# Performance work log

Measured on AMD Instinct MI355X. Metric: run time of the kernel, lower is better.

Reference implementation:

```python
import jax, jax.numpy as jnp
import numpy as np

B, T, I, H, TGT = 256, 4096, 8, 32, 8


def setup_inputs() -> dict:
    key = jax.random.key(0)
    ks = jax.random.split(key, 6)
    return {
        "inputs": jax.random.normal(ks[0], (B, T, I), jnp.float32),
        "encode_weights": jax.random.normal(ks[1], (H, I), jnp.float32) * 0.3,   # xavier-ish
        "w_ih": jax.random.normal(ks[2], (3 * H, H), jnp.float32) * 0.1,        # GRU weight_ih_l0
        "w_hh": jax.random.normal(ks[3], (3 * H, H), jnp.float32) * 0.1,        # GRU weight_hh_l0
        "b_ih": jax.random.normal(ks[4], (3 * H,), jnp.float32) * 0.1,
        "b_hh": jax.random.normal(ks[5], (3 * H,), jnp.float32) * 0.1,
    }


def _gru(gx_t, w_hh, b_hh, h0):
    # gx_t: time-major input-gate pre-activations [T, B, 3H]; PyTorch GRU math:
    # r = sig(gx_r + gh_r); z = sig(gx_z + gh_z); n = tanh(gx_n + r*gh_n); h = (1-z)*n + z*h
    Hd = h0.shape[-1]
    def step(h, gx):
        gh = h @ w_hh.T + b_hh                      # [B, 3H]
        r = jax.nn.sigmoid(gx[..., :Hd] + gh[..., :Hd])
        z = jax.nn.sigmoid(gx[..., Hd:2 * Hd] + gh[..., Hd:2 * Hd])
        n = jnp.tanh(gx[..., 2 * Hd:] + r * gh[..., 2 * Hd:])
        h_new = (1.0 - z) * n + z * h
        return h_new, h_new
    _, hs = jax.lax.scan(step, h0, gx_t)            # hs: [T, B, H]
    return hs


def reference(inputs, encode_weights, w_ih, w_hh, b_ih, b_hh):
    # encode = F.linear(inputs, encode_weights)
    encode = jnp.einsum('bti,hi->bth', inputs, encode_weights)      # [B, T, H]
    gx = jnp.einsum('bth,gh->btg', encode, w_ih) + b_ih             # [B, T, 3H]
    gx_t = jnp.swapaxes(gx, 0, 1)                                   # [T, B, 3H]
    h0 = jnp.zeros((inputs.shape[0], encode_weights.shape[0]), inputs.dtype)
    latents = jnp.swapaxes(_gru(gx_t, w_hh, b_hh, h0), 0, 1)        # [B, T, H]
    # tied decoder: F.linear(latents, encode_weights[:, :target_size].T)
    outputs = jnp.einsum('bth,ho->bto', latents, encode_weights[:, :TGT])
    return outputs, latents
```

## Files before the change

kernel.cpp:

```cpp
#include <hip/hip_runtime.h>
#include <hip/hip_bf16.h>
#include <cstdint>
#include <cstddef>

#define Bsz  256
#define Tn   4096
#define In   8
#define Hn   32
#define TGTn 8

#define ALPHA (-1.44269504088896341f)
#define BETA  ( 2.88539008177792682f)

#if __has_builtin(__builtin_amdgcn_exp2f)
__device__ __forceinline__ float exp2f_fast(float x) { return __builtin_amdgcn_exp2f(x); }
#else
__device__ __forceinline__ float exp2f_fast(float x) { return __expf(x * 0.69314718056f); }
#endif
__device__ __forceinline__ float rcpf(float x) { return __builtin_amdgcn_rcpf(x); }

__device__ __forceinline__ float half_sum(float x) {
    auto r = __builtin_amdgcn_permlane32_swap(__float_as_int(x), __float_as_int(x),
                                              false, false);
    return __int_as_float((int)r[0]) + __int_as_float((int)r[1]);
}

__global__ void fuse_wih_kernel(const float* __restrict__ w_ih,
                                const float* __restrict__ E,
                                float* __restrict__ Wf) {
    int tid = threadIdx.x;
    int g = tid >> 3, i = tid & 7;
    float acc = 0.f;
#pragma unroll
    for (int k = 0; k < Hn; ++k)
        acc = fmaf(w_ih[g * Hn + k], E[k * In + i], acc);
    Wf[g * In + i] = acc;
}

#define GRU_STEP(XA, XB, XRA, XRB, DO_REFILL)                                        \
  {                                                                                  \
             \
    float ar = br_h, az = bz_h, anx = bxn_f, anh = bhn_h;                            \
    ar  = fmaf(XA.x, wxr0, ar);  ar  = fmaf(XA.y, wxr1, ar);                         \
    ar  = fmaf(XA.z, wxr2, ar);  ar  = fmaf(XA.w, wxr3, ar);                         \
    ar  = fmaf(XB.x, wxr4, ar);  ar  = fmaf(XB.y, wxr5, ar);                         \
    ar  = fmaf(XB.z, wxr6, ar);  ar  = fmaf(XB.w, wxr7, ar);                         \
    az  = fmaf(XA.x, wxz0, az);  az  = fmaf(XA.y, wxz1, az);                         \
    az  = fmaf(XA.z, wxz2, az);  az  = fmaf(XA.w, wxz3, az);                         \
    az  = fmaf(XB.x, wxz4, az);  az  = fmaf(XB.y, wxz5, az);                         \
    az  = fmaf(XB.z, wxz6, az);  az  = fmaf(XB.w, wxz7, az);                         \
    anx = fmaf(XA.x, wxn0, anx); anx = fmaf(XA.y, wxn1, anx);                        \
    anx = fmaf(XA.z, wxn2, anx); anx = fmaf(XA.w, wxn3, anx);                        \
    anx = fmaf(XB.x, wxn4, anx); anx = fmaf(XB.y, wxn5, anx);                        \
    anx = fmaf(XB.z, wxn6, anx); anx = fmaf(XB.w, wxn7, anx);                        \
                                                    \
    ar = fmaf(H0,  wr0,  ar);  az = fmaf(H0,  wz0,  az);  anh = fmaf(H0,  wn0,  anh);\
    ar = fmaf(H1,  wr1,  ar);  az = fmaf(H1,  wz1,  az);  anh = fmaf(H1,  wn1,  anh);\
    ar = fmaf(H2,  wr2,  ar);  az = fmaf(H2,  wz2,  az);  anh = fmaf(H2,  wn2,  anh);\
    ar = fmaf(H3,  wr3,  ar);  az = fmaf(H3,  wz3,  az);  anh = fmaf(H3,  wn3,  anh);\
    ar = fmaf(H4,  wr4,  ar);  az = fmaf(H4,  wz4,  az);  anh = fmaf(H4,  wn4,  anh);\
    ar = fmaf(H5,  wr5,  ar);  az = fmaf(H5,  wz5,  az);  anh = fmaf(H5,  wn5,  anh);\
    ar = fmaf(H6,  wr6,  ar);  az = fmaf(H6,  wz6,  az);  anh = fmaf(H6,  wn6,  anh);\
    ar = fmaf(H7,  wr7,  ar);  az = fmaf(H7,  wz7,  az);  anh = fmaf(H7,  wn7,  anh);\
    ar = fmaf(H8,  wr8,  ar);  az = fmaf(H8,  wz8,  az);  anh = fmaf(H8,  wn8,  anh);\
    ar = fmaf(H9,  wr9,  ar);  az = fmaf(H9,  wz9,  az);  anh = fmaf(H9,  wn9,  anh);\
    ar = fmaf(H10, wr10, ar);  az = fmaf(H10, wz10, az);  anh = fmaf(H10, wn10, anh);\
    ar = fmaf(H11, wr11, ar);  az = fmaf(H11, wz11, az);  anh = fmaf(H11, wn11, anh);\
    ar = fmaf(H12, wr12, ar);  az = fmaf(H12, wz12, az);  anh = fmaf(H12, wn12, anh);\
    ar = fmaf(H13, wr13, ar);  az = fmaf(H13, wz13, az);  anh = fmaf(H13, wn13, anh);\
    ar = fmaf(H14, wr14, ar);  az = fmaf(H14, wz14, az);  anh = fmaf(H14, wn14, anh);\
    ar = fmaf(H15, wr15, ar);  az = fmaf(H15, wz15, az);  anh = fmaf(H15, wn15, anh);\
    float cr  = half_sum(ar);                           \
    float cz  = half_sum(az);                                                        \
    float chn = half_sum(anh);                          \
    float r = rcpf(1.f + exp2f_fast(cr));                                            \
    float z = rcpf(1.f + exp2f_fast(cz));                                            \
    float e = exp2f_fast(__builtin_fmaf(r, chn, anx));                               \
    float u = rcpf(e + 1.f);                                                         \
    float n = __builtin_fmaf(-2.f, u, 1.f);                                          \
    hj = __builtin_fmaf(z, hj - n, n);                                               \
    lds_h[j] = hj;                               \
    latb_u[j] = hj;                                                                  \
    latb_u += Hn;                                               \
    if (DO_REFILL) {                                                                 \
        XRA = *(const float4*)refp;                                                  \
        XRB = *(const float4*)(refp + 4);                                            \
        refp += In;                                             \
    }                                                                                \
               \
    {                                                                                \
        float4 q0 = *(const float4*)&lds_h[grp * 16 + 0];                            \
        float4 q1 = *(const float4*)&lds_h[grp * 16 + 4];                            \
        float4 q2 = *(const float4*)&lds_h[grp * 16 + 8];                            \
        float4 q3 = *(const float4*)&lds_h[grp * 16 + 12];                           \
        H0  = q0.x; H1  = q0.y; H2  = q0.z; H3  = q0.w;                              \
        H4  = q1.x; H5  = q1.y; H6  = q1.z; H7  = q1.w;                              \
        H8  = q2.x; H9  = q2.y; H10 = q2.z; H11 = q2.w;                              \
        H12 = q3.x; H13 = q3.y; H14 = q3.z; H15 = q3.w;                              \
    }                                                                                \
  }

#define KEEP(v) asm volatile("" : "+v"(v))
__attribute__((amdgpu_flat_work_group_size(64, 64), amdgpu_waves_per_eu(1, 1)))
__global__ void gru_kernel(const float* __restrict__ x,
                           const float* __restrict__ Wf,
                           const float* __restrict__ w_hh,
                           const float* __restrict__ b_ih,
                           const float* __restrict__ b_hh,
                           float* __restrict__ latents) {
    __shared__ __align__(16) float lds_h[Hn];

    const int lane = threadIdx.x & 63;
    const int grp  = lane >> 5;
    const int j    = lane & 31;
    const int b    = blockIdx.x;

    float wr0,wr1,wr2,wr3,wr4,wr5,wr6,wr7,wr8,wr9,wr10,wr11,wr12,wr13,wr14,wr15;
    float wz0,wz1,wz2,wz3,wz4,wz5,wz6,wz7,wz8,wz9,wz10,wz11,wz12,wz13,wz14,wz15;
    float wn0,wn1,wn2,wn3,wn4,wn5,wn6,wn7,wn8,wn9,wn10,wn11,wn12,wn13,wn14,wn15;
#define LOADW(M)                                                                  \
    {                                                                             \
        const int c = grp * 16 + M;                                               \
        wr##M = ALPHA * w_hh[(0*Hn + j)*Hn + c];                                  \
        wz##M = ALPHA * w_hh[(1*Hn + j)*Hn + c];                                  \
        wn##M = BETA  * w_hh[(2*Hn + j)*Hn + c];                                  \
        KEEP(wr##M); KEEP(wz##M); KEEP(wn##M);                                    \
    }
    LOADW(0) LOADW(1) LOADW(2)  LOADW(3)  LOADW(4)  LOADW(5)  LOADW(6)  LOADW(7)
    LOADW(8) LOADW(9) LOADW(10) LOADW(11) LOADW(12) LOADW(13) LOADW(14) LOADW(15)
#undef LOADW

    float wxr0,wxr1,wxr2,wxr3,wxr4,wxr5,wxr6,wxr7;
    float wxz0,wxz1,wxz2,wxz3,wxz4,wxz5,wxz6,wxz7;
    float wxn0,wxn1,wxn2,wxn3,wxn4,wxn5,wxn6,wxn7;
#define LOADX(I)                                                                  \
    wxr##I = 0.5f * ALPHA * Wf[(0*Hn + j)*In + I];                                \
    wxz##I = 0.5f * ALPHA * Wf[(1*Hn + j)*In + I];                                \
    wxn##I = BETA         * Wf[(2*Hn + j)*In + I];                                \
    KEEP(wxr##I); KEEP(wxz##I); KEEP(wxn##I);
    LOADX(0) LOADX(1) LOADX(2) LOADX(3) LOADX(4) LOADX(5) LOADX(6) LOADX(7)
#undef LOADX

    float br_h  = 0.5f * ALPHA * (b_ih[j]        + b_hh[j]);
    float bz_h  = 0.5f * ALPHA * (b_ih[Hn + j]   + b_hh[Hn + j]);
    float bxn_f = BETA * b_ih[2*Hn + j];
    float bhn_h = 0.5f * BETA * b_hh[2*Hn + j];
    KEEP(br_h); KEEP(bz_h); KEEP(bxn_f); KEEP(bhn_h);

    const float* xb   = x + (size_t)b * Tn * In;
    float* latb_u     = latents + (size_t)b * Tn * Hn;
    const float* refp = xb + 4 * In;

    float hj = 0.f;
    float H0=0.f,H1=0.f,H2=0.f,H3=0.f,H4=0.f,H5=0.f,H6=0.f,H7=0.f,
          H8=0.f,H9=0.f,H10=0.f,H11=0.f,H12=0.f,H13=0.f,H14=0.f,H15=0.f;

    float4 a0 = *(const float4*)&xb[0*In], b0 = *(const float4*)&xb[0*In + 4];
    float4 a1 = *(const float4*)&xb[1*In], b1 = *(const float4*)&xb[1*In + 4];
    float4 a2 = *(const float4*)&xb[2*In], b2 = *(const float4*)&xb[2*In + 4];
    float4 a3 = *(const float4*)&xb[3*In], b3 = *(const float4*)&xb[3*In + 4];

#pragma unroll 1
    for (int s0 = 0; s0 < Tn - 4; s0 += 4) {
        GRU_STEP(a0, b0, a0, b0, true)
        GRU_STEP(a1, b1, a1, b1, true)
        GRU_STEP(a2, b2, a2, b2, true)
        GRU_STEP(a3, b3, a3, b3, true)
    }
    GRU_STEP(a0, b0, a0, b0, false)
    GRU_STEP(a1, b1, a1, b1, false)
    GRU_STEP(a2, b2, a2, b2, false)
    GRU_STEP(a3, b3, a3, b3, false)
}
#undef KEEP

__global__ void decode_kernel(const float* __restrict__ lat,
                              const float* __restrict__ E,
                              float* __restrict__ out) {
    __shared__ float ldsE[Hn * TGTn];
    int tid = threadIdx.x;
    if (tid < Hn * TGTn) ldsE[tid] = E[tid];
    __syncthreads();
    size_t idx = (size_t)blockIdx.x * 256 + tid;
    int o      = (int)(idx & (TGTn - 1));
    size_t row = idx >> 3;
    const float* lrow = lat + row * Hn;
    float acc = 0.f;
#pragma unroll
    for (int h = 0; h < Hn; ++h)
        acc = fmaf(lrow[h], ldsE[h * TGTn + o], acc);
    out[idx] = acc;
}

extern "C" void kernel_launch(void* const* d_in, const int* in_sizes, int n_in,
                              void* d_out, int out_size, void* d_ws, size_t ws_size,
                              hipStream_t stream) {
    const float* x    = (const float*)d_in[0];
    const float* E    = (const float*)d_in[1];
    const float* w_ih = (const float*)d_in[2];
    const float* w_hh = (const float*)d_in[3];
    const float* b_ih = (const float*)d_in[4];
    const float* b_hh = (const float*)d_in[5];

    float* out = (float*)d_out;
    float* lat = out + (size_t)Bsz * Tn * TGTn;
    float* Wf  = (float*)d_ws;

    fuse_wih_kernel<<<1, 768, 0, stream>>>(w_ih, E, Wf);
    gru_kernel<<<Bsz, 64, 0, stream>>>(x, Wf, w_hh, b_ih, b_hh, lat);
    decode_kernel<<<(Bsz * Tn * TGTn) / 256, 256, 0, stream>>>(lat, E, out);
}
```

Measured before the change: 1.143 ms.

## Replace LDS hidden-state broadcast with DPP row-rotate FMAs and permlane swaps

The per-step hidden-state exchange no longer goes through shared memory (an LDS write followed by four float4 reads). Each lane now holds one hidden value and the recurrent matvec uses v_fmac_f32 with DPP row_ror operands, so the value moves across lanes inside the FMA. Lanes are remapped and the w_hh weights are pre-permuted to match, with permlane16/permlane32 swaps doing the reductions and the redistribution of h. This targets LDS latency on the serial critical path of the recurrence, at the cost of inline asm with hand-placed s_nop hazards and a tricky lane mapping that could be wrong.

```diff
diff --git a/kernel.cpp b/kernel.cpp
--- a/kernel.cpp
+++ b/kernel.cpp
@@ -19,11 +19,26 @@
 #endif
 __device__ __forceinline__ float rcpf(float x) { return __builtin_amdgcn_rcpf(x); }
 
-__device__ __forceinline__ float half_sum(float x) {
-    auto r = __builtin_amdgcn_permlane32_swap(__float_as_int(x), __float_as_int(x),
+template<int N>
+__device__ __forceinline__ float dpp_ror(float x) {
+    int xi = __float_as_int(x);
+    int r = __builtin_amdgcn_update_dpp(xi, xi, 0x120 + N, 0xF, 0xF, false);
+    return __int_as_float(r);
+}
+
+__device__ __forceinline__ float halfsum16(float x) {
+    auto r = __builtin_amdgcn_permlane16_swap(__float_as_int(x), __float_as_int(x),
                                               false, false);
     return __int_as_float((int)r[0]) + __int_as_float((int)r[1]);
 }
+
+#define FMAC_DPP(acc, h, w, N)                                                       \
+    asm volatile("v_fmac_f32 %0, %1, %2 row_ror:" #N " row_mask:0xf bank_mask:0xf"   \
+                 : "+v"(acc) : "v"(h), "v"(w))
+#define FMAC_DPP_FIRST(acc, h, w, N)                                                 \
+    asm volatile("s_nop 1\n\t"                                                       \
+                 "v_fmac_f32 %0, %1, %2 row_ror:" #N " row_mask:0xf bank_mask:0xf"   \
+                 : "+v"(acc) : "v"(h), "v"(w))
 
 __global__ void fuse_wih_kernel(const float* __restrict__ w_ih,
                                 const float* __restrict__ E,
@@ -37,9 +52,14 @@
     Wf[g * In + i] = acc;
 }
 
+#define HROT3(N)                                                                     \
+    FMAC_DPP(ar,  hsrc, whr##N, N);                                                  \
+    FMAC_DPP(az,  hsrc, whz##N, N);                                                  \
+    FMAC_DPP(anh, hsrc, whn##N, N);
+
 #define GRU_STEP(XA, XB, XRA, XRB, DO_REFILL)                                        \
   {                                                                                  \
-             \
+                       \
     float ar = br_h, az = bz_h, anx = bxn_f, anh = bhn_h;                            \
     ar  = fmaf(XA.x, wxr0, ar);  ar  = fmaf(XA.y, wxr1, ar);                         \
     ar  = fmaf(XA.z, wxr2, ar);  ar  = fmaf(XA.w, wxr3, ar);                         \
@@ -53,50 +73,39 @@
     anx = fmaf(XA.z, wxn2, anx); anx = fmaf(XA.w, wxn3, anx);                        \
     anx = fmaf(XB.x, wxn4, anx); anx = fmaf(XB.y, wxn5, anx);                        \
     anx = fmaf(XB.z, wxn6, anx); anx = fmaf(XB.w, wxn7, anx);                        \
-                                                    \
-    ar = fmaf(H0,  wr0,  ar);  az = fmaf(H0,  wz0,  az);  anh = fmaf(H0,  wn0,  anh);\
-    ar = fmaf(H1,  wr1,  ar);  az = fmaf(H1,  wz1,  az);  anh = fmaf(H1,  wn1,  anh);\
-    ar = fmaf(H2,  wr2,  ar);  az = fmaf(H2,  wz2,  az);  anh = fmaf(H2,  wn2,  anh);\
-    ar = fmaf(H3,  wr3,  ar);  az = fmaf(H3,  wz3,  az);  anh = fmaf(H3,  wn3,  anh);\
-    ar = fmaf(H4,  wr4,  ar);  az = fmaf(H4,  wz4,  az);  anh = fmaf(H4,  wn4,  anh);\
-    ar = fmaf(H5,  wr5,  ar);  az = fmaf(H5,  wz5,  az);  anh = fmaf(H5,  wn5,  anh);\
-    ar = fmaf(H6,  wr6,  ar);  az = fmaf(H6,  wz6,  az);  anh = fmaf(H6,  wn6,  anh);\
-    ar = fmaf(H7,  wr7,  ar);  az = fmaf(H7,  wz7,  az);  anh = fmaf(H7,  wn7,  anh);\
-    ar = fmaf(H8,  wr8,  ar);  az = fmaf(H8,  wz8,  az);  anh = fmaf(H8,  wn8,  anh);\
-    ar = fmaf(H9,  wr9,  ar);  az = fmaf(H9,  wz9,  az);  anh = fmaf(H9,  wn9,  anh);\
-    ar = fmaf(H10, wr10, ar);  az = fmaf(H10, wz10, az);  anh = fmaf(H10, wn10, anh);\
-    ar = fmaf(H11, wr11, ar);  az = fmaf(H11, wz11, az);  anh = fmaf(H11, wn11, anh);\
-    ar = fmaf(H12, wr12, ar);  az = fmaf(H12, wz12, az);  anh = fmaf(H12, wn12, anh);\
-    ar = fmaf(H13, wr13, ar);  az = fmaf(H13, wz13, az);  anh = fmaf(H13, wn13, anh);\
-    ar = fmaf(H14, wr14, ar);  az = fmaf(H14, wz14, az);  anh = fmaf(H14, wn14, anh);\
-    ar = fmaf(H15, wr15, ar);  az = fmaf(H15, wz15, az);  anh = fmaf(H15, wn15, anh);\
-    float cr  = half_sum(ar);                           \
-    float cz  = half_sum(az);                                                        \
-    float chn = half_sum(anh);                          \
+            \
+    ar  = fmaf(hsrc, whr0, ar);                                                      \
+    az  = fmaf(hsrc, whz0, az);                                                      \
+    anh = fmaf(hsrc, whn0, anh);                                                     \
+    FMAC_DPP_FIRST(ar, hsrc, whr1, 1);                                               \
+    FMAC_DPP(az,  hsrc, whz1, 1);                                                    \
+    FMAC_DPP(anh, hsrc, whn1, 1);                                                    \
+    HROT3(2)  HROT3(3)  HROT3(4)  HROT3(5)  HROT3(6)  HROT3(7)  HROT3(8)             \
+    HROT3(9)  HROT3(10) HROT3(11) HROT3(12) HROT3(13) HROT3(14) HROT3(15)            \
+    float cr  = halfsum16(ar);                           \
+    float cz  = halfsum16(az);                                                       \
+    float chn = halfsum16(anh);                          \
     float r = rcpf(1.f + exp2f_fast(cr));                                            \
     float z = rcpf(1.f + exp2f_fast(cz));                                            \
     float e = exp2f_fast(__builtin_fmaf(r, chn, anx));                               \
     float u = rcpf(e + 1.f);                                                         \
     float n = __builtin_fmaf(-2.f, u, 1.f);                                          \
     hj = __builtin_fmaf(z, hj - n, n);                                               \
-    lds_h[j] = hj;                               \
-    latb_u[j] = hj;                                                                  \
+               \
+    {                                                                                \
+        auto rr = __builtin_amdgcn_permlane32_swap(__float_as_int(hj),               \
+                                                   __float_as_int(hj),               \
+                                                   false, false);                    \
+        float s0 = __int_as_float((int)rr[0]);                                       \
+        float s1 = __int_as_float((int)rr[1]);                                       \
+        hsrc = pickr1 ? s1 : s0;                                                     \
+    }                                                                                \
+    latb_u[j] = hj;                            \
     latb_u += Hn;                                               \
     if (DO_REFILL) {                                                                 \
         XRA = *(const float4*)refp;                                                  \
         XRB = *(const float4*)(refp + 4);                                            \
         refp += In;                                             \
-    }                                                                                \
-               \
-    {                                                                                \
-        float4 q0 = *(const float4*)&lds_h[grp * 16 + 0];                            \
-        float4 q1 = *(const float4*)&lds_h[grp * 16 + 4];                            \
-        float4 q2 = *(const float4*)&lds_h[grp * 16 + 8];                            \
-        float4 q3 = *(const float4*)&lds_h[grp * 16 + 12];                           \
-        H0  = q0.x; H1  = q0.y; H2  = q0.z; H3  = q0.w;                              \
-        H4  = q1.x; H5  = q1.y; H6  = q1.z; H7  = q1.w;                              \
-        H8  = q2.x; H9  = q2.y; H10 = q2.z; H11 = q2.w;                              \
-        H12 = q3.x; H13 = q3.y; H14 = q3.z; H15 = q3.w;                              \
     }                                                                                \
   }
 
@@ -108,23 +117,45 @@
                            const float* __restrict__ b_ih,
                            const float* __restrict__ b_hh,
                            float* __restrict__ latents) {
-    __shared__ __align__(16) float lds_h[Hn];
-
-    const int lane = threadIdx.x & 63;
-    const int grp  = lane >> 5;
-    const int j    = lane & 31;
-    const int b    = blockIdx.x;
-
-    float wr0,wr1,wr2,wr3,wr4,wr5,wr6,wr7,wr8,wr9,wr10,wr11,wr12,wr13,wr14,wr15;
-    float wz0,wz1,wz2,wz3,wz4,wz5,wz6,wz7,wz8,wz9,wz10,wz11,wz12,wz13,wz14,wz15;
-    float wn0,wn1,wn2,wn3,wn4,wn5,wn6,wn7,wn8,wn9,wn10,wn11,wn12,wn13,wn14,wn15;
+    const int lane   = threadIdx.x & 63;
+    const int rowpar = (lane >> 4) & 1;
+    const int j      = (lane & 15) | ((lane >> 1) & 16);
+    const int b      = blockIdx.x;
+
+    int rho[16];
+    {
+        float q = (float)(lane & 15);
+        rho[0]  = lane & 15;
+        rho[1]  = (int)dpp_ror<1>(q);   rho[2]  = (int)dpp_ror<2>(q);
+        rho[3]  = (int)dpp_ror<3>(q);   rho[4]  = (int)dpp_ror<4>(q);
+        rho[5]  = (int)dpp_ror<5>(q);   rho[6]  = (int)dpp_ror<6>(q);
+        rho[7]  = (int)dpp_ror<7>(q);   rho[8]  = (int)dpp_ror<8>(q);
+        rho[9]  = (int)dpp_ror<9>(q);   rho[10] = (int)dpp_ror<10>(q);
+        rho[11] = (int)dpp_ror<11>(q);  rho[12] = (int)dpp_ror<12>(q);
+        rho[13] = (int)dpp_ror<13>(q);  rho[14] = (int)dpp_ror<14>(q);
+        rho[15] = (int)dpp_ror<15>(q);
+    }
+    bool pickr1;
+    {
+        float t = (float)lane;
+        auto rr = __builtin_amdgcn_permlane32_swap(__float_as_int(t),
+                                                   __float_as_int(t),
+                                                   false, false);
+        bool r0_own    = ((int)__int_as_float((int)rr[0]) == lane);
+        bool use_swap  = (rowpar != ((lane >> 5) & 1));
+        pickr1 = (use_swap == r0_own);
+    }
+
+    float whr0,whr1,whr2,whr3,whr4,whr5,whr6,whr7,whr8,whr9,whr10,whr11,whr12,whr13,whr14,whr15;
+    float whz0,whz1,whz2,whz3,whz4,whz5,whz6,whz7,whz8,whz9,whz10,whz11,whz12,whz13,whz14,whz15;
+    float whn0,whn1,whn2,whn3,whn4,whn5,whn6,whn7,whn8,whn9,whn10,whn11,whn12,whn13,whn14,whn15;
 #define LOADW(M)                                                                  \
     {                                                                             \
-        const int c = grp * 16 + M;                                               \
-        wr##M = ALPHA * w_hh[(0*Hn + j)*Hn + c];                                  \
-        wz##M = ALPHA * w_hh[(1*Hn + j)*Hn + c];                                  \
-        wn##M = BETA  * w_hh[(2*Hn + j)*Hn + c];                                  \
-        KEEP(wr##M); KEEP(wz##M); KEEP(wn##M);                                    \
+        const int c = rowpar * 16 + rho[M];                                       \
+        whr##M = ALPHA * w_hh[(0*Hn + j)*Hn + c];                                 \
+        whz##M = ALPHA * w_hh[(1*Hn + j)*Hn + c];                                 \
+        whn##M = BETA  * w_hh[(2*Hn + j)*Hn + c];                                 \
+        KEEP(whr##M); KEEP(whz##M); KEEP(whn##M);                                 \
     }
     LOADW(0) LOADW(1) LOADW(2)  LOADW(3)  LOADW(4)  LOADW(5)  LOADW(6)  LOADW(7)
     LOADW(8) LOADW(9) LOADW(10) LOADW(11) LOADW(12) LOADW(13) LOADW(14) LOADW(15)
@@ -152,8 +183,7 @@
     const float* refp = xb + 4 * In;
 
     float hj = 0.f;
-    float H0=0.f,H1=0.f,H2=0.f,H3=0.f,H4=0.f,H5=0.f,H6=0.f,H7=0.f,
-          H8=0.f,H9=0.f,H10=0.f,H11=0.f,H12=0.f,H13=0.f,H14=0.f,H15=0.f;
+    float hsrc = 0.f;
 
     float4 a0 = *(const float4*)&xb[0*In], b0 = *(const float4*)&xb[0*In + 4];
     float4 a1 = *(const float4*)&xb[1*In], b1 = *(const float4*)&xb[1*In + 4];
```

New measurement: 959.6 us, median of 2. 16.1% less time.

## Map two batch rows per wave with full-length hidden dot per lane

Applied to the files above, without the earlier changes.

Each wave now processes two batch elements: a 32-lane half per row, with each lane computing the full 32-wide recurrent dot product for its hidden unit. This removes the permlane32 swap half-sum reduction from every step. The input-gate pre-activation for the next step is computed after the hidden-state store, taking it off the recurrence's critical path. In exchange each lane issues twice as many recurrent FMAs and LDS reads per step, holds twice as many weight registers, and only half as many workgroups are launched.

```diff
diff --git a/kernel.cpp b/kernel.cpp
--- a/kernel.cpp
+++ b/kernel.cpp
@@ -18,12 +18,6 @@
 __device__ __forceinline__ float exp2f_fast(float x) { return __expf(x * 0.69314718056f); }
 #endif
 __device__ __forceinline__ float rcpf(float x) { return __builtin_amdgcn_rcpf(x); }
-
-__device__ __forceinline__ float half_sum(float x) {
-    auto r = __builtin_amdgcn_permlane32_swap(__float_as_int(x), __float_as_int(x),
-                                              false, false);
-    return __int_as_float((int)r[0]) + __int_as_float((int)r[1]);
-}
 
 __global__ void fuse_wih_kernel(const float* __restrict__ w_ih,
                                 const float* __restrict__ E,
@@ -37,70 +31,73 @@
     Wf[g * In + i] = acc;
 }
 
-#define GRU_STEP(XA, XB, XRA, XRB, DO_REFILL)                                        \
+#define KEEP(v) asm volatile("" : "+v"(v))
+
+#define H_FMA(K)                                                                     \
+    ar  = fmaf(H##K, wr##K, ar);                                                     \
+    az  = fmaf(H##K, wz##K, az);                                                     \
+    anh = fmaf(H##K, wn##K, anh);
+
+#define RELOAD_H()                                                                   \
   {                                                                                  \
-             \
-    float ar = br_h, az = bz_h, anx = bxn_f, anh = bhn_h;                            \
-    ar  = fmaf(XA.x, wxr0, ar);  ar  = fmaf(XA.y, wxr1, ar);                         \
-    ar  = fmaf(XA.z, wxr2, ar);  ar  = fmaf(XA.w, wxr3, ar);                         \
-    ar  = fmaf(XB.x, wxr4, ar);  ar  = fmaf(XB.y, wxr5, ar);                         \
-    ar  = fmaf(XB.z, wxr6, ar);  ar  = fmaf(XB.w, wxr7, ar);                         \
-    az  = fmaf(XA.x, wxz0, az);  az  = fmaf(XA.y, wxz1, az);                         \
-    az  = fmaf(XA.z, wxz2, az);  az  = fmaf(XA.w, wxz3, az);                         \
-    az  = fmaf(XB.x, wxz4, az);  az  = fmaf(XB.y, wxz5, az);                         \
-    az  = fmaf(XB.z, wxz6, az);  az  = fmaf(XB.w, wxz7, az);                         \
-    anx = fmaf(XA.x, wxn0, anx); anx = fmaf(XA.y, wxn1, anx);                        \
-    anx = fmaf(XA.z, wxn2, anx); anx = fmaf(XA.w, wxn3, anx);                        \
-    anx = fmaf(XB.x, wxn4, anx); anx = fmaf(XB.y, wxn5, anx);                        \
-    anx = fmaf(XB.z, wxn6, anx); anx = fmaf(XB.w, wxn7, anx);                        \
-                                                    \
-    ar = fmaf(H0,  wr0,  ar);  az = fmaf(H0,  wz0,  az);  anh = fmaf(H0,  wn0,  anh);\
-    ar = fmaf(H1,  wr1,  ar);  az = fmaf(H1,  wz1,  az);  anh = fmaf(H1,  wn1,  anh);\
-    ar = fmaf(H2,  wr2,  ar);  az = fmaf(H2,  wz2,  az);  anh = fmaf(H2,  wn2,  anh);\
-    ar = fmaf(H3,  wr3,  ar);  az = fmaf(H3,  wz3,  az);  anh = fmaf(H3,  wn3,  anh);\
-    ar = fmaf(H4,  wr4,  ar);  az = fmaf(H4,  wz4,  az);  anh = fmaf(H4,  wn4,  anh);\
-    ar = fmaf(H5,  wr5,  ar);  az = fmaf(H5,  wz5,  az);  anh = fmaf(H5,  wn5,  anh);\
-    ar = fmaf(H6,  wr6,  ar);  az = fmaf(H6,  wz6,  az);  anh = fmaf(H6,  wn6,  anh);\
-    ar = fmaf(H7,  wr7,  ar);  az = fmaf(H7,  wz7,  az);  anh = fmaf(H7,  wn7,  anh);\
-    ar = fmaf(H8,  wr8,  ar);  az = fmaf(H8,  wz8,  az);  anh = fmaf(H8,  wn8,  anh);\
-    ar = fmaf(H9,  wr9,  ar);  az = fmaf(H9,  wz9,  az);  anh = fmaf(H9,  wn9,  anh);\
-    ar = fmaf(H10, wr10, ar);  az = fmaf(H10, wz10, az);  anh = fmaf(H10, wn10, anh);\
-    ar = fmaf(H11, wr11, ar);  az = fmaf(H11, wz11, az);  anh = fmaf(H11, wn11, anh);\
-    ar = fmaf(H12, wr12, ar);  az = fmaf(H12, wz12, az);  anh = fmaf(H12, wn12, anh);\
-    ar = fmaf(H13, wr13, ar);  az = fmaf(H13, wz13, az);  anh = fmaf(H13, wn13, anh);\
-    ar = fmaf(H14, wr14, ar);  az = fmaf(H14, wz14, az);  anh = fmaf(H14, wn14, anh);\
-    ar = fmaf(H15, wr15, ar);  az = fmaf(H15, wz15, az);  anh = fmaf(H15, wn15, anh);\
-    float cr  = half_sum(ar);                           \
-    float cz  = half_sum(az);                                                        \
-    float chn = half_sum(anh);                          \
-    float r = rcpf(1.f + exp2f_fast(cr));                                            \
-    float z = rcpf(1.f + exp2f_fast(cz));                                            \
-    float e = exp2f_fast(__builtin_fmaf(r, chn, anx));                               \
+    float4 q0 = *(const float4*)&lds_h[hbase + 0];                                   \
+    float4 q1 = *(const float4*)&lds_h[hbase + 4];                                   \
+    float4 q2 = *(const float4*)&lds_h[hbase + 8];                                   \
+    float4 q3 = *(const float4*)&lds_h[hbase + 12];                                  \
+    float4 q4 = *(const float4*)&lds_h[hbase + 16];                                  \
+    float4 q5 = *(const float4*)&lds_h[hbase + 20];                                  \
+    float4 q6 = *(const float4*)&lds_h[hbase + 24];                                  \
+    float4 q7 = *(const float4*)&lds_h[hbase + 28];                                  \
+    H0 =q0.x; H1 =q0.y; H2 =q0.z; H3 =q0.w;  H4 =q1.x; H5 =q1.y; H6 =q1.z; H7 =q1.w; \
+    H8 =q2.x; H9 =q2.y; H10=q2.z; H11=q2.w;  H12=q3.x; H13=q3.y; H14=q3.z; H15=q3.w; \
+    H16=q4.x; H17=q4.y; H18=q4.z; H19=q4.w;  H20=q5.x; H21=q5.y; H22=q5.z; H23=q5.w; \
+    H24=q6.x; H25=q6.y; H26=q6.z; H27=q6.w;  H28=q7.x; H29=q7.y; H30=q7.z; H31=q7.w; \
+  }
+
+#define PREACT(XA, XB)                                                               \
+  {                                                                                  \
+    axr = br_s;                                                                      \
+    axr = fmaf(XA.x, wxr0, axr); axr = fmaf(XA.y, wxr1, axr);                        \
+    axr = fmaf(XA.z, wxr2, axr); axr = fmaf(XA.w, wxr3, axr);                        \
+    axr = fmaf(XB.x, wxr4, axr); axr = fmaf(XB.y, wxr5, axr);                        \
+    axr = fmaf(XB.z, wxr6, axr); axr = fmaf(XB.w, wxr7, axr);                        \
+    axz = bz_s;                                                                      \
+    axz = fmaf(XA.x, wxz0, axz); axz = fmaf(XA.y, wxz1, axz);                        \
+    axz = fmaf(XA.z, wxz2, axz); axz = fmaf(XA.w, wxz3, axz);                        \
+    axz = fmaf(XB.x, wxz4, axz); axz = fmaf(XB.y, wxz5, axz);                        \
+    axz = fmaf(XB.z, wxz6, axz); axz = fmaf(XB.w, wxz7, axz);                        \
+    axn = bxn_s;                                                                     \
+    axn = fmaf(XA.x, wxn0, axn); axn = fmaf(XA.y, wxn1, axn);                        \
+    axn = fmaf(XA.z, wxn2, axn); axn = fmaf(XA.w, wxn3, axn);                        \
+    axn = fmaf(XB.x, wxn4, axn); axn = fmaf(XB.y, wxn5, axn);                        \
+    axn = fmaf(XB.z, wxn6, axn); axn = fmaf(XB.w, wxn7, axn);                        \
+  }
+
+#define GRU_STEP(XNA, XNB, XRA, XRB, DO_REFILL)                                      \
+  {                                                                                  \
+    float ar = axr, az = axz, anh = bhn_s, anx = axn;                                \
+    H_FMA(0)  H_FMA(1)  H_FMA(2)  H_FMA(3)  H_FMA(4)  H_FMA(5)  H_FMA(6)  H_FMA(7)  \
+    H_FMA(8)  H_FMA(9)  H_FMA(10) H_FMA(11) H_FMA(12) H_FMA(13) H_FMA(14) H_FMA(15) \
+    H_FMA(16) H_FMA(17) H_FMA(18) H_FMA(19) H_FMA(20) H_FMA(21) H_FMA(22) H_FMA(23) \
+    H_FMA(24) H_FMA(25) H_FMA(26) H_FMA(27) H_FMA(28) H_FMA(29) H_FMA(30) H_FMA(31) \
+    float r = rcpf(1.f + exp2f_fast(ar));                                            \
+    float z = rcpf(1.f + exp2f_fast(az));                                            \
+    float e = exp2f_fast(__builtin_fmaf(r, anh, anx));                               \
     float u = rcpf(e + 1.f);                                                         \
     float n = __builtin_fmaf(-2.f, u, 1.f);                                          \
     hj = __builtin_fmaf(z, hj - n, n);                                               \
-    lds_h[j] = hj;                               \
-    latb_u[j] = hj;                                                                  \
-    latb_u += Hn;                                               \
+    lds_h[lane] = hj;                          \
+    *latp = hj;                                                                      \
+    latp += Hn;                                                                      \
+    RELOAD_H()                                       \
+    PREACT(XNA, XNB)                                           \
     if (DO_REFILL) {                                                                 \
         XRA = *(const float4*)refp;                                                  \
         XRB = *(const float4*)(refp + 4);                                            \
-        refp += In;                                             \
-    }                                                                                \
-               \
-    {                                                                                \
-        float4 q0 = *(const float4*)&lds_h[grp * 16 + 0];                            \
-        float4 q1 = *(const float4*)&lds_h[grp * 16 + 4];                            \
-        float4 q2 = *(const float4*)&lds_h[grp * 16 + 8];                            \
-        float4 q3 = *(const float4*)&lds_h[grp * 16 + 12];                           \
-        H0  = q0.x; H1  = q0.y; H2  = q0.z; H3  = q0.w;                              \
-        H4  = q1.x; H5  = q1.y; H6  = q1.z; H7  = q1.w;                              \
-        H8  = q2.x; H9  = q2.y; H10 = q2.z; H11 = q2.w;                              \
-        H12 = q3.x; H13 = q3.y; H14 = q3.z; H15 = q3.w;                              \
+        refp += In;                                                                  \
     }                                                                                \
   }
 
-#define KEEP(v) asm volatile("" : "+v"(v))
 __attribute__((amdgpu_flat_work_group_size(64, 64), amdgpu_waves_per_eu(1, 1)))
 __global__ void gru_kernel(const float* __restrict__ x,
                            const float* __restrict__ Wf,
@@ -108,69 +105,89 @@
                            const float* __restrict__ b_ih,
                            const float* __restrict__ b_hh,
                            float* __restrict__ latents) {
-    __shared__ __align__(16) float lds_h[Hn];
-
-    const int lane = threadIdx.x & 63;
-    const int grp  = lane >> 5;
-    const int j    = lane & 31;
-    const int b    = blockIdx.x;
-
-    float wr0,wr1,wr2,wr3,wr4,wr5,wr6,wr7,wr8,wr9,wr10,wr11,wr12,wr13,wr14,wr15;
-    float wz0,wz1,wz2,wz3,wz4,wz5,wz6,wz7,wz8,wz9,wz10,wz11,wz12,wz13,wz14,wz15;
-    float wn0,wn1,wn2,wn3,wn4,wn5,wn6,wn7,wn8,wn9,wn10,wn11,wn12,wn13,wn14,wn15;
-#define LOADW(M)                                                                  \
+    __shared__ __align__(16) float lds_h[2 * Hn];
+
+    const int lane  = threadIdx.x & 63;
+    const int bsel  = lane >> 5;
+    const int j     = lane & 31;
+    const int hbase = bsel * Hn;
+    const int b     = blockIdx.x * 2 + bsel;
+
+    float wr0,wr1,wr2,wr3,wr4,wr5,wr6,wr7,wr8,wr9,wr10,wr11,wr12,wr13,wr14,wr15,
+          wr16,wr17,wr18,wr19,wr20,wr21,wr22,wr23,wr24,wr25,wr26,wr27,wr28,wr29,wr30,wr31;
+    float wz0,wz1,wz2,wz3,wz4,wz5,wz6,wz7,wz8,wz9,wz10,wz11,wz12,wz13,wz14,wz15,
+          wz16,wz17,wz18,wz19,wz20,wz21,wz22,wz23,wz24,wz25,wz26,wz27,wz28,wz29,wz30,wz31;
+    float wn0,wn1,wn2,wn3,wn4,wn5,wn6,wn7,wn8,wn9,wn10,wn11,wn12,wn13,wn14,wn15,
+          wn16,wn17,wn18,wn19,wn20,wn21,wn22,wn23,wn24,wn25,wn26,wn27,wn28,wn29,wn30,wn31;
+#define LW(P, G, S, Q, N0, N1, N2, N3)                                            \
     {                                                                             \
-        const int c = grp * 16 + M;                                               \
-        wr##M = ALPHA * w_hh[(0*Hn + j)*Hn + c];                                  \
-        wz##M = ALPHA * w_hh[(1*Hn + j)*Hn + c];                                  \
-        wn##M = BETA  * w_hh[(2*Hn + j)*Hn + c];                                  \
-        KEEP(wr##M); KEEP(wz##M); KEEP(wn##M);                                    \
+        float4 q = *(const float4*)&w_hh[((G)*Hn + j)*Hn + 4*(Q)];                \
+        P##N0 = (S)*q.x; P##N1 = (S)*q.y; P##N2 = (S)*q.z; P##N3 = (S)*q.w;       \
+        KEEP(P##N0); KEEP(P##N1); KEEP(P##N2); KEEP(P##N3);                       \
     }
-    LOADW(0) LOADW(1) LOADW(2)  LOADW(3)  LOADW(4)  LOADW(5)  LOADW(6)  LOADW(7)
-    LOADW(8) LOADW(9) LOADW(10) LOADW(11) LOADW(12) LOADW(13) LOADW(14) LOADW(15)
-#undef LOADW
+    LW(wr,0,ALPHA,0, 0,1,2,3)     LW(wr,0,ALPHA,1, 4,5,6,7)
+    LW(wr,0,ALPHA,2, 8,9,10,11)   LW(wr,0,ALPHA,3, 12,13,14,15)
+    LW(wr,0,ALPHA,4, 16,17,18,19) LW(wr,0,ALPHA,5, 20,21,22,23)
+    LW(wr,0,ALPHA,6, 24,25,26,27) LW(wr,0,ALPHA,7, 28,29,30,31)
+    LW(wz,1,ALPHA,0, 0,1,2,3)     LW(wz,1,ALPHA,1, 4,5,6,7)
+    LW(wz,1,ALPHA,2, 8,9,10,11)   LW(wz,1,ALPHA,3, 12,13,14,15)
+    LW(wz,1,ALPHA,4, 16,17,18,19) LW(wz,1,ALPHA,5, 20,21,22,23)
+    LW(wz,1,ALPHA,6, 24,25,26,27) LW(wz,1,ALPHA,7, 28,29,30,31)
+    LW(wn,2,BETA,0, 0,1,2,3)      LW(wn,2,BETA,1, 4,5,6,7)
+    LW(wn,2,BETA,2, 8,9,10,11)    LW(wn,2,BETA,3, 12,13,14,15)
+    LW(wn,2,BETA,4, 16,17,18,19)  LW(wn,2,BETA,5, 20,21,22,23)
+    LW(wn,2,BETA,6, 24,25,26,27)  LW(wn,2,BETA,7, 28,29,30,31)
+#undef LW
 
     float wxr0,wxr1,wxr2,wxr3,wxr4,wxr5,wxr6,wxr7;
     float wxz0,wxz1,wxz2,wxz3,wxz4,wxz5,wxz6,wxz7;
     float wxn0,wxn1,wxn2,wxn3,wxn4,wxn5,wxn6,wxn7;
-#define LOADX(I)                                                                  \
-    wxr##I = 0.5f * ALPHA * Wf[(0*Hn + j)*In + I];                                \
-    wxz##I = 0.5f * ALPHA * Wf[(1*Hn + j)*In + I];                                \
-    wxn##I = BETA         * Wf[(2*Hn + j)*In + I];                                \
-    KEEP(wxr##I); KEEP(wxz##I); KEEP(wxn##I);
-    LOADX(0) LOADX(1) LOADX(2) LOADX(3) LOADX(4) LOADX(5) LOADX(6) LOADX(7)
-#undef LOADX
-
-    float br_h  = 0.5f * ALPHA * (b_ih[j]        + b_hh[j]);
-    float bz_h  = 0.5f * ALPHA * (b_ih[Hn + j]   + b_hh[Hn + j]);
-    float bxn_f = BETA * b_ih[2*Hn + j];
-    float bhn_h = 0.5f * BETA * b_hh[2*Hn + j];
-    KEEP(br_h); KEEP(bz_h); KEEP(bxn_f); KEEP(bhn_h);
+#define LX(P, G, S, Q, N0, N1, N2, N3)                                            \
+    {                                                                             \
+        float4 q = *(const float4*)&Wf[((G)*Hn + j)*In + 4*(Q)];                  \
+        P##N0 = (S)*q.x; P##N1 = (S)*q.y; P##N2 = (S)*q.z; P##N3 = (S)*q.w;       \
+        KEEP(P##N0); KEEP(P##N1); KEEP(P##N2); KEEP(P##N3);                       \
+    }
+    LX(wxr,0,ALPHA,0, 0,1,2,3) LX(wxr,0,ALPHA,1, 4,5,6,7)
+    LX(wxz,1,ALPHA,0, 0,1,2,3) LX(wxz,1,ALPHA,1, 4,5,6,7)
+    LX(wxn,2,BETA,0, 0,1,2,3)  LX(wxn,2,BETA,1, 4,5,6,7)
+#undef LX
+
+    float br_s  = ALPHA * (b_ih[j]        + b_hh[j]);
+    float bz_s  = ALPHA * (b_ih[Hn + j]   + b_hh[Hn + j]);
+    float bxn_s = BETA  *  b_ih[2*Hn + j];
+    float bhn_s = BETA  *  b_hh[2*Hn + j];
+    KEEP(br_s); KEEP(bz_s); KEEP(bxn_s); KEEP(bhn_s);
 
     const float* xb   = x + (size_t)b * Tn * In;
-    float* latb_u     = latents + (size_t)b * Tn * Hn;
+    float* latp       = latents + (size_t)b * Tn * Hn + j;
     const float* refp = xb + 4 * In;
 
     float hj = 0.f;
     float H0=0.f,H1=0.f,H2=0.f,H3=0.f,H4=0.f,H5=0.f,H6=0.f,H7=0.f,
-          H8=0.f,H9=0.f,H10=0.f,H11=0.f,H12=0.f,H13=0.f,H14=0.f,H15=0.f;
+          H8=0.f,H9=0.f,H10=0.f,H11=0.f,H12=0.f,H13=0.f,H14=0.f,H15=0.f,
+          H16=0.f,H17=0.f,H18=0.f,H19=0.f,H20=0.f,H21=0.f,H22=0.f,H23=0.f,
+          H24=0.f,H25=0.f,H26=0.f,H27=0.f,H28=0.f,H29=0.f,H30=0.f,H31=0.f;
 
     float4 a0 = *(const float4*)&xb[0*In], b0 = *(const float4*)&xb[0*In + 4];
     float4 a1 = *(const float4*)&xb[1*In], b1 = *(const float4*)&xb[1*In + 4];
     float4 a2 = *(const float4*)&xb[2*In], b2 = *(const float4*)&xb[2*In + 4];
     float4 a3 = *(const float4*)&xb[3*In], b3 = *(const float4*)&xb[3*In + 4];
 
+    float axr, axz, axn;
+    PREACT(a0, b0)
+
 #pragma unroll 1
     for (int s0 = 0; s0 < Tn - 4; s0 += 4) {
-        GRU_STEP(a0, b0, a0, b0, true)
-        GRU_STEP(a1, b1, a1, b1, true)
-        GRU_STEP(a2, b2, a2, b2, true)
-        GRU_STEP(a3, b3, a3, b3, true)
+        GRU_STEP(a1, b1, a0, b0, true)
+        GRU_STEP(a2, b2, a1, b1, true)
+        GRU_STEP(a3, b3, a2, b2, true)
+        GRU_STEP(a0, b0, a3, b3, true)
     }
-    GRU_STEP(a0, b0, a0, b0, false)
-    GRU_STEP(a1, b1, a1, b1, false)
-    GRU_STEP(a2, b2, a2, b2, false)
-    GRU_STEP(a3, b3, a3, b3, false)
+    GRU_STEP(a1, b1, a0, b0, false)
+    GRU_STEP(a2, b2, a1, b1, false)
+    GRU_STEP(a3, b3, a2, b2, false)
+    GRU_STEP(a0, b0, a3, b3, false)
 }
 #undef KEEP
 
@@ -207,6 +224,6 @@
     float* Wf  = (float*)d_ws;
 
     fuse_wih_kernel<<<1, 768, 0, stream>>>(w_ih, E, Wf);
-    gru_kernel<<<Bsz, 64, 0, stream>>>(x, Wf, w_hh, b_ih, b_hh, lat);
+    gru_kernel<<<Bsz / 2, 64, 0, stream>>>(x, Wf, w_hh, b_ih, b_hh, lat);
     decode_kernel<<<(Bsz * Tn * TGTn) / 256, 256, 0, stream>>>(lat, E, out);
 }
```

New measurement: 1.239 ms. 1.08x slower.
